# Performance work log

Hardware: AMD Instinct MI355X
Metric: run time of the kernel (lower is better)

Reference implementation:

```python
import jax, jax.numpy as jnp
import numpy as np

NUM_HEADS = 16
NEG_INF = -9e15


def setup_inputs() -> dict:
    key = jax.random.key(0)
    k1, k2, k3 = jax.random.split(key, 3)
    B, S, D = 2, 2048, 1024
    # xavier-uniform-ish init scale for weights
    lim_qkv = float(np.sqrt(6.0 / (D + 3 * D)))
    lim_o = float(np.sqrt(6.0 / (D + D)))
    return {
        "x": jax.random.normal(k1, (B, S, D), dtype=jnp.float32),
        "w_qkv": jax.random.uniform(k2, (3 * D, D), minval=-lim_qkv, maxval=lim_qkv, dtype=jnp.float32),
        "b_qkv": jnp.zeros((3 * D,), dtype=jnp.float32),
        "w_o": jax.random.uniform(k3, (D, D), minval=-lim_o, maxval=lim_o, dtype=jnp.float32),
        "b_o": jnp.zeros((D,), dtype=jnp.float32),
    }


def reference(x, w_qkv, b_qkv, w_o, b_o):
    B, S, D = x.shape
    H = NUM_HEADS
    hd = D // H
    # qkv projection: [B,S,3D]
    qkv = x @ w_qkv.T + b_qkv
    # -> [B, H, S, 3*hd], then split
    qkv = qkv.reshape(B, S, H, 3 * hd).transpose(0, 2, 1, 3)
    q, k, v = jnp.split(qkv, 3, axis=-1)  # each [B,H,S,hd]
    scale = 1.0 / jnp.sqrt(jnp.asarray(hd, dtype=x.dtype))
    logits = jnp.einsum("bhqd,bhkd->bhqk", q, k) * scale
    attn = jax.nn.softmax(logits, axis=-1)
    vals = jnp.einsum("bhqk,bhkd->bhqd", attn, v)
    vals = vals.transpose(0, 2, 1, 3).reshape(B, S, D)
    return vals @ w_o.T + b_o
```

## Files before the change

kernel.cpp:

```cpp
#include <hip/hip_runtime.h>
#include <math.h>

#define NHEADS 16
#define HD 64

typedef __attribute__((ext_vector_type(8))) _Float16 half8;
typedef __attribute__((ext_vector_type(4))) _Float16 half4;
typedef __attribute__((ext_vector_type(4))) float f32x4;
typedef __attribute__((ext_vector_type(16))) float f32x16;
typedef __attribute__((ext_vector_type(4))) unsigned int u32x4;

__device__ inline void load_lds16(const void* g, void* l) {
    __builtin_amdgcn_global_load_lds(
        (const __attribute__((address_space(1))) unsigned int*)g,
        (__attribute__((address_space(3))) unsigned int*)l, 16, 0, 0);
}
__device__ inline void pl32swap(unsigned int& x, unsigned int& y) {
    asm volatile("v_permlane32_swap_b32 %0, %1" : "+v"(x), "+v"(y));
}

#define NX  4194304
#define NWQ 3145728
#define NWO 1048576
__global__ void cvt_all(const float* __restrict__ x, const float* __restrict__ wq,
                        const float* __restrict__ wo, _Float16* __restrict__ xf,
                        _Float16* __restrict__ wqf, _Float16* __restrict__ wof) {
    int i = (blockIdx.x * blockDim.x + threadIdx.x) * 8;
    const float* src; _Float16* dst; int off;
    if (i < NX)            { src = x;  dst = xf;  off = i; }
    else if (i < NX + NWQ) { src = wq; dst = wqf; off = i - NX; }
    else                   { src = wo; dst = wof; off = i - (NX + NWQ); }
    float4 a = *(const float4*)(src + off);
    float4 b = *(const float4*)(src + off + 4);
    half8 h;
    h[0] = (_Float16)a.x; h[1] = (_Float16)a.y; h[2] = (_Float16)a.z; h[3] = (_Float16)a.w;
    h[4] = (_Float16)b.x; h[5] = (_Float16)b.y; h[6] = (_Float16)b.z; h[7] = (_Float16)b.w;
    *(half8*)(dst + off) = h;
}

#define QSCALE 0.18033688f
__global__ __launch_bounds__(512, 2) void gemm_qkv(
    const _Float16* __restrict__ A, const _Float16* __restrict__ B,
    const float* __restrict__ bias,
    _Float16* __restrict__ Qf, _Float16* __restrict__ Kf,
    _Float16* __restrict__ VfT) {
    __shared__ __align__(1024) unsigned char smem[114688];
    const int tid = threadIdx.x;
    const int l = tid & 63, w = tid >> 6;
    const int wr = w >> 2, wc = w & 3;
    const int col16 = l & 15, kc = l >> 4;
    const int bid = blockIdx.y * gridDim.x + blockIdx.x;
    const int swz = (bid & 7) * 32 + (bid >> 3);
    const int m0 = (swz >> 4) * 256, n0 = (swz & 15) * 192;

    const int srcRow = w * 8 + (l >> 3);
    const int srcChunk = ((l & 7) ^ (l >> 3)) * 8;
    size_t aSrc[4], bSrc[3];
    #pragma unroll
    for (int q = 0; q < 4; ++q)
        aSrc[q] = (size_t)(m0 + q * 64 + srcRow) * 1024 + srcChunk;
    #pragma unroll
    for (int q = 0; q < 3; ++q)
        bSrc[q] = (size_t)(n0 + q * 64 + srcRow) * 1024 + srcChunk;
    const int ldsLane = w * 1024;

    const int swzl = col16 & 7;
    const int chOff0 = ((kc) ^ swzl) << 4;
    const int chOff1 = ((4 + kc) ^ swzl) << 4;
    int rowA[8], rowB[3];
    #pragma unroll
    for (int f = 0; f < 8; ++f) rowA[f] = (wr * 128 + f * 16 + col16) * 128;
    #pragma unroll
    for (int g = 0; g < 3; ++g) rowB[g] = (wc * 48 + g * 16 + col16) * 128;

    f32x4 acc[8][3] = {};

#define SU_A(q_, tt_) load_lds16(A + aSrc[q_] + (tt_) * 64, \
        smem + ((tt_) & 1) * 32768 + (q_) * 8192 + ldsLane);
#define SU_B(q_, tt_) load_lds16(B + bSrc[q_] + (tt_) * 64, \
        smem + 65536 + ((tt_) & 1) * 24576 + (q_) * 8192 + ldsLane);

#define VMW2 asm volatile("s_waitcnt vmcnt(2)" ::: "memory");
#define VMW3 asm volatile("s_waitcnt vmcnt(3)" ::: "memory");
#define VMW0 asm volatile("s_waitcnt vmcnt(0)" ::: "memory");

#define PH(mh_, g0_, gn_, bufA_, bufB_, VMWSTMT, STAGES) { \
    VMWSTMT \
    __builtin_amdgcn_sched_barrier(0); \
    __builtin_amdgcn_s_barrier(); \
    __builtin_amdgcn_sched_barrier(0); \
    half8 af[4][2], bf[gn_][2]; \
    _Pragma("unroll") \
    for (int f = 0; f < 4; ++f) { \
        const unsigned char* ap = smem + (bufA_) + rowA[(mh_) * 4 + f]; \
        af[f][0] = *(const half8*)(ap + chOff0); \
        af[f][1] = *(const half8*)(ap + chOff1); \
    } \
    _Pragma("unroll") \
    for (int g = 0; g < (gn_); ++g) { \
        const unsigned char* bp = smem + (bufB_) + rowB[(g0_) + g]; \
        bf[g][0] = *(const half8*)(bp + chOff0); \
        bf[g][1] = *(const half8*)(bp + chOff1); \
    } \
    STAGES \
    asm volatile("s_waitcnt lgkmcnt(0)" ::: "memory"); \
    __builtin_amdgcn_sched_barrier(0); \
    __builtin_amdgcn_s_setprio(1); \
    _Pragma("unroll") \
    for (int f = 0; f < 4; ++f) \
        _Pragma("unroll") \
        for (int g = 0; g < (gn_); ++g) { \
            acc[(mh_) * 4 + f][(g0_) + g] = __builtin_amdgcn_mfma_f32_16x16x32_f16( \
                af[f][0], bf[g][0], acc[(mh_) * 4 + f][(g0_) + g], 0, 0, 0); \
            acc[(mh_) * 4 + f][(g0_) + g] = __builtin_amdgcn_mfma_f32_16x16x32_f16( \
                af[f][1], bf[g][1], acc[(mh_) * 4 + f][(g0_) + g], 0, 0, 0); \
        } \
    __builtin_amdgcn_s_setprio(0); }

    SU_B(0, 0) SU_B(1, 0) SU_B(2, 0)
    SU_A(0, 0) SU_A(2, 0) SU_A(1, 0) SU_A(3, 0)

    for (int t = 0; t < 15; ++t) {
        const int bufA = (t & 1) * 32768;
        const int bufB = 65536 + (t & 1) * 24576;
        PH(0, 0, 2, bufA, bufB, VMW2, { SU_B(0, t + 1) SU_B(1, t + 1) })
        PH(0, 2, 1, bufA, bufB, ,     { SU_B(2, t + 1) })
        PH(1, 0, 2, bufA, bufB, VMW3, { SU_A(0, t + 1) SU_A(2, t + 1) })
        PH(1, 2, 1, bufA, bufB, ,     { SU_A(1, t + 1) SU_A(3, t + 1) })
    }
    PH(0, 0, 2, 32768, 65536 + 24576, VMW2, {})
    PH(0, 2, 1, 32768, 65536 + 24576, ,     {})
    PH(1, 0, 2, 32768, 65536 + 24576, VMW0, {})
    PH(1, 2, 1, 32768, 65536 + 24576, ,     {})

#undef SU_A
#undef SU_B
#undef VMW2
#undef VMW3
#undef VMW0
#undef PH

    const int rowb = m0 + wr * 128 + (l >> 4) * 4;
    const int colb = n0 + wc * 48 + col16;
    #pragma unroll
    for (int n = 0; n < 3; ++n) {
        int col = colb + n * 16;
        int h = col / 192;
        int rem = col - h * 192;
        int part = rem >> 6, d = rem & 63;
        float bv = bias[col];
        #pragma unroll
        for (int m = 0; m < 8; ++m) {
            int r0 = rowb + m * 16;
            int b = r0 >> 11, s0r = r0 & 2047;
            int bh = b * 16 + h;
            if (part == 0) {
                #pragma unroll
                for (int j = 0; j < 4; ++j)
                    Qf[((size_t)bh * 2048 + s0r + j) * 64 + d] =
                        (_Float16)((acc[m][n][j] + bv) * QSCALE);
            } else if (part == 1) {
                #pragma unroll
                for (int j = 0; j < 4; ++j)
                    Kf[((size_t)bh * 2048 + s0r + j) * 64 + d] = (_Float16)(acc[m][n][j] + bv);
            } else {
                half4 pk;
                pk[0] = (_Float16)(acc[m][n][0] + bv);
                pk[1] = (_Float16)(acc[m][n][1] + bv);
                pk[2] = (_Float16)(acc[m][n][2] + bv);
                pk[3] = (_Float16)(acc[m][n][3] + bv);
                *(half4*)&VfT[((size_t)bh * 64 + d) * 2048 + s0r] = pk;
            }
        }
    }
}

__global__ __launch_bounds__(256, 2) void gemm_o(
    const _Float16* __restrict__ A, const _Float16* __restrict__ B,
    const float* __restrict__ bias, float* __restrict__ C,
    int M, int N, int K) {
    __shared__ __align__(1024) unsigned char smem[36864];
    const int tid = threadIdx.x;
    const int l = tid & 63, w = tid >> 6;
    const int wr = w >> 1, wc = w & 1;
    const int nwg = gridDim.x * gridDim.y;
    const int bid = blockIdx.y * gridDim.x + blockIdx.x;
    const int swz = (bid & 7) * (nwg >> 3) + (bid >> 3);
    const int m0 = (swz / gridDim.x) * 128, n0 = (swz % gridDim.x) * 64;
    const int srow = tid >> 2;
    const int schunk = (tid & 3) ^ ((srow >> 1) & 3);
    const size_t gA0 = (size_t)(m0 + srow) * K + schunk * 8;
    const size_t gA1 = gA0 + (size_t)64 * K;
    const size_t gB0 = (size_t)(n0 + srow) * K + schunk * 8;
    unsigned char* ldsW = smem + w * 1024;
    const int col16 = l & 15, kc = l >> 4;
    const int ra0 = wr * 64 + col16;
    const int offA = ra0 * 64 + ((kc ^ ((ra0 >> 1) & 3)) * 16);
    const int rb0 = wc * 32 + col16;
    const int offB = rb0 * 64 + ((kc ^ ((rb0 >> 1) & 3)) * 16);
    f32x4 acc[4][2] = {};

#define OSTAGE(k0_, buf_)                                                              \
    load_lds16(A + gA0 + (k0_), ldsW + (buf_) * 12288 + 0);                            \
    load_lds16(A + gA1 + (k0_), ldsW + (buf_) * 12288 + 4096);                         \
    load_lds16(B + gB0 + (k0_), ldsW + (buf_) * 12288 + 8192);
#define OSTEP(s_, buf_, VM, dostage)                                                   \
    asm volatile("s_waitcnt " VM ::: "memory");                                        \
    __builtin_amdgcn_sched_barrier(0);                                                 \
    __builtin_amdgcn_s_barrier();                                                      \
    if (dostage) { OSTAGE(((s_) + 2) * 32, ((buf_) + 2) % 3) }                         \
    {                                                                                  \
        const unsigned char* bs = smem + (buf_) * 12288;                               \
        half8 af[4], bf[2];                                                            \
        _Pragma("unroll")                                                              \
        for (int m = 0; m < 4; ++m) af[m] = *(const half8*)(bs + offA + m * 1024);     \
        _Pragma("unroll")                                                              \
        for (int n = 0; n < 2; ++n) bf[n] = *(const half8*)(bs + 8192 + offB + n * 1024); \
        _Pragma("unroll")                                                              \
        for (int m = 0; m < 4; ++m)                                                    \
            _Pragma("unroll")                                                          \
            for (int n = 0; n < 2; ++n)                                                \
                acc[m][n] = __builtin_amdgcn_mfma_f32_16x16x32_f16(af[m], bf[n], acc[m][n], 0, 0, 0); \
    }

    OSTAGE(0, 0)
    OSTAGE(32, 1)
    for (int t = 0; t < 30; t += 3) {
        OSTEP(t, 0, "vmcnt(3)", 1)
        OSTEP(t + 1, 1, "vmcnt(3)", 1)
        OSTEP(t + 2, 2, "vmcnt(3)", 1)
    }
    OSTEP(30, 0, "vmcnt(3)", 0)
    OSTEP(31, 1, "vmcnt(0)", 0)
#undef OSTAGE
#undef OSTEP

    const int rowb = m0 + wr * 64 + (l >> 4) * 4;
    const int colb = n0 + wc * 32 + col16;
    float bv[2];
    #pragma unroll
    for (int n = 0; n < 2; ++n) bv[n] = bias[colb + n * 16];
    #pragma unroll
    for (int m = 0; m < 4; ++m)
        #pragma unroll
        for (int j = 0; j < 4; ++j) {
            float* crow = C + (size_t)(rowb + m * 16 + j) * N + colb;
            #pragma unroll
            for (int n = 0; n < 2; ++n) crow[n * 16] = acc[m][n][j] + bv[n];
        }
}

__global__ __launch_bounds__(512, 2) void mfma_attn(
    const _Float16* __restrict__ Qf, const _Float16* __restrict__ Kf,
    const _Float16* __restrict__ VfT, _Float16* __restrict__ vals) {
    __shared__ __align__(1024) unsigned char smem[49152];
    const int tid = threadIdx.x;
    const int l = tid & 63, w = tid >> 6;
    const int l31 = l & 31, hl = l >> 5;
    const int hwbid = blockIdx.y * gridDim.x + blockIdx.x;
    const int q_t = (hwbid >> 3) & 7;
    const int bh = (hwbid & 7) + ((hwbid >> 6) << 3);
    const int q0 = q_t * 256;
    const int h = bh & 15, b = bh >> 4;

    half8 qf[4];
    {
        const _Float16* qp = Qf + ((size_t)bh * 2048 + q0 + w * 32 + l31) * 64 + hl * 8;
        #pragma unroll
        for (int c = 0; c < 4; ++c) qf[c] = *(const half8*)(qp + c * 16);
    }
    f32x16 zvec = {};
    f32x16 o0 = {}, o1 = {};
    float mshift = 0.f, lsum = 0.f;

    const _Float16* Kg = Kf + (size_t)bh * 2048 * 64;
    const _Float16* Vg = VfT + (size_t)bh * 64 * 2048;

    int offK, offV;
    {
        int row2 = w * 4 + (l >> 4);
        int slot = (l & 15) ^ (row2 & 15);
        int row = row2 * 2 + (slot >> 3);
        int chunk = slot & 7;
        offK = row * 64 + chunk * 8;
        offV = row * 2048 + chunk * 8;
    }
    const int sbase = (l31 & 1) * 8;
    const int xr = (l31 >> 1) & 15;
    const int rb0 = (l31 >> 1) * 256;

    #define STAGE(kt0, buf)                                                            \
        {                                                                              \
            unsigned char* bK = smem + (buf) * 8192 + w * 1024;                        \
            unsigned char* bV = smem + 24576 + (buf) * 8192 + w * 1024;                \
            load_lds16(Kg + (size_t)(kt0) * 64 + offK, bK);                            \
            load_lds16(Vg + (kt0) + offV, bV);                                         \
        }

    #define QK_TILE(kb, D0, D1)                                                        \
        {                                                                              \
            const unsigned char* Ksb_ = smem + (kb) * 8192;                            \
            {                                                                          \
                int chOff = ((sbase + hl) ^ xr) << 4;                                  \
                half8 k0_ = *(const half8*)(Ksb_ + rb0 + chOff);                       \
                half8 k1_ = *(const half8*)(Ksb_ + rb0 + 4096 + chOff);                \
                D0 = __builtin_amdgcn_mfma_f32_32x32x16_f16(k0_, qf[0], zvec, 0, 0, 0);\
                D1 = __builtin_amdgcn_mfma_f32_32x32x16_f16(k1_, qf[0], zvec, 0, 0, 0);\
            }                                                                          \
            _Pragma("unroll")                                                          \
            for (int kcq = 1; kcq < 4; ++kcq) {                                        \
                int chOff = ((sbase + kcq * 2 + hl) ^ xr) << 4;                        \
                half8 k0_ = *(const half8*)(Ksb_ + rb0 + chOff);                       \
                half8 k1_ = *(const half8*)(Ksb_ + rb0 + 4096 + chOff);                \
                D0 = __builtin_amdgcn_mfma_f32_32x32x16_f16(k0_, qf[kcq], D0, 0, 0, 0);\
                D1 = __builtin_amdgcn_mfma_f32_32x32x16_f16(k1_, qf[kcq], D1, 0, 0, 0);\
            }                                                                          \
        }

    #define SMPV(S0, S1, vb_)                                                          \
        {                                                                              \
            const unsigned char* Vsb_ = smem + 24576 + (vb_) * 8192;                   \
            if (__any(mshift != 0.f)) {                                                \
                _Pragma("unroll")                                                      \
                for (int r = 0; r < 16; ++r) { S0[r] -= mshift; S1[r] -= mshift; }     \
            }                                                                          \
            float r0 = 0.f, r1 = 0.f, r2 = 0.f, r3 = 0.f;                              \
            unsigned int a[2][8];                                                      \
            _Pragma("unroll")                                                          \
            for (int j = 0; j < 8; ++j) {                                              \
                float p0 = __builtin_amdgcn_exp2f(S0[2 * j]);                          \
                float p1 = __builtin_amdgcn_exp2f(S0[2 * j + 1]);                      \
                float q0_ = __builtin_amdgcn_exp2f(S1[2 * j]);                         \
                float q1_ = __builtin_amdgcn_exp2f(S1[2 * j + 1]);                     \
                r0 += p0; r1 += p1; r2 += q0_; r3 += q1_;                              \
                a[0][j] = __builtin_bit_cast(unsigned int, __builtin_amdgcn_cvt_pkrtz(p0, p1));   \
                a[1][j] = __builtin_bit_cast(unsigned int, __builtin_amdgcn_cvt_pkrtz(q0_, q1_)); \
            }                                                                          \
            float rsum = (r0 + r1) + (r2 + r3);                                        \
            if (__any(rsum > 32768.f)) {                                               \
                float pmax = S0[0];                                                    \
                _Pragma("unroll")                                                      \
                for (int r = 1; r < 16; ++r) pmax = fmaxf(pmax, S0[r]);                \
                _Pragma("unroll")                                                      \
                for (int r = 0; r < 16; ++r) pmax = fmaxf(pmax, S1[r]);                \
                pmax = fmaxf(pmax, __shfl_xor(pmax, 32, 64));                          \
                float d_ = fmaxf(pmax, 0.f);                                           \
                float corr = __builtin_amdgcn_exp2f(-d_);                              \
                _Pragma("unroll")                                                      \
                for (int r = 0; r < 16; ++r) { S0[r] -= d_; S1[r] -= d_; }             \
                _Pragma("unroll")                                                      \
                for (int r = 0; r < 16; ++r) { o0[r] *= corr; o1[r] *= corr; }         \
                lsum *= corr;                                                          \
                mshift += d_;                                                          \
                r0 = r1 = r2 = r3 = 0.f;                                               \
                _Pragma("unroll")                                                      \
                for (int j = 0; j < 8; ++j) {                                          \
                    float p0 = __builtin_amdgcn_exp2f(S0[2 * j]);                      \
                    float p1 = __builtin_amdgcn_exp2f(S0[2 * j + 1]);                  \
                    float q0_ = __builtin_amdgcn_exp2f(S1[2 * j]);                     \
                    float q1_ = __builtin_amdgcn_exp2f(S1[2 * j + 1]);                 \
                    r0 += p0; r1 += p1; r2 += q0_; r3 += q1_;                          \
                    a[0][j] = __builtin_bit_cast(unsigned int, __builtin_amdgcn_cvt_pkrtz(p0, p1));   \
                    a[1][j] = __builtin_bit_cast(unsigned int, __builtin_amdgcn_cvt_pkrtz(q0_, q1_)); \
                }                                                                      \
                rsum = (r0 + r1) + (r2 + r3);                                          \
            }                                                                          \
            lsum += rsum;                                                              \
            _Pragma("unroll")                                                          \
            for (int c = 0; c < 2; ++c) {                                              \
                pl32swap(a[c][0], a[c][2]);                                            \
                pl32swap(a[c][1], a[c][3]);                                            \
                pl32swap(a[c][4], a[c][6]);                                            \
                pl32swap(a[c][5], a[c][7]);                                            \
            }                                                                          \
            _Pragma("unroll")                                                          \
            for (int kk = 0; kk < 4; ++kk) {                                           \
                u32x4 pw;                                                              \
                pw.x = a[kk >> 1][(kk & 1) * 4 + 0];                                   \
                pw.y = a[kk >> 1][(kk & 1) * 4 + 1];                                   \
                pw.z = a[kk >> 1][(kk & 1) * 4 + 2];                                   \
                pw.w = a[kk >> 1][(kk & 1) * 4 + 3];                                   \
                half8 pf = __builtin_bit_cast(half8, pw);                              \
                int chOff = ((sbase + kk * 2 + hl) ^ xr) << 4;                         \
                half8 v0 = *(const half8*)(Vsb_ + rb0 + chOff);                        \
                half8 v1 = *(const half8*)(Vsb_ + rb0 + 4096 + chOff);                 \
                o0 = __builtin_amdgcn_mfma_f32_32x32x16_f16(v0, pf, o0, 0, 0, 0);      \
                o1 = __builtin_amdgcn_mfma_f32_32x32x16_f16(v1, pf, o1, 0, 0, 0);      \
            }                                                                          \
        }

    #define AITER(tt, kb, VM, dostage)                                                 \
        asm volatile("s_waitcnt " VM ::: "memory");                                    \
        __builtin_amdgcn_sched_barrier(0);                                             \
        __builtin_amdgcn_s_barrier();                                                  \
        if (dostage) STAGE(((tt) + 2) * 64, ((kb) + 2) % 3)                            \
        QK_TILE(kb, sS0, sS1)                                                          \
        SMPV(sS0, sS1, kb)

    STAGE(0, 0)
    STAGE(64, 1)
    f32x16 sS0, sS1;
    for (int t = 0; t < 30; t += 3) {
        AITER(t, 0, "vmcnt(2)", 1)
        AITER(t + 1, 1, "vmcnt(2)", 1)
        AITER(t + 2, 2, "vmcnt(2)", 1)
    }
    AITER(30, 0, "vmcnt(2)", 0)
    AITER(31, 1, "vmcnt(0)", 0)

    lsum += __shfl_xor(lsum, 32, 64);
    float inv = 1.f / lsum;
    size_t orow = ((size_t)(b * 2048 + q0 + w * 32 + l31)) * 1024 + h * 64;
    #pragma unroll
    for (int dc = 0; dc < 2; ++dc) {
        const f32x16* op = dc ? &o1 : &o0;
        #pragma unroll
        for (int rq = 0; rq < 4; ++rq) {
            int d0 = dc * 32 + rq * 8 + hl * 4;
            half4 hv;
            #pragma unroll
            for (int j = 0; j < 4; ++j) hv[j] = (_Float16)((*op)[rq * 4 + j] * inv);
            *(half4*)(vals + orow + d0) = hv;
        }
    }
}

extern "C" void kernel_launch(void* const* d_in, const int* in_sizes, int n_in,
                              void* d_out, int out_size, void* d_ws, size_t ws_size,
                              hipStream_t stream) {
    const float* x     = (const float*)d_in[0];
    const float* w_qkv = (const float*)d_in[1];
    const float* b_qkv = (const float*)d_in[2];
    const float* w_o   = (const float*)d_in[3];
    const float* b_o   = (const float*)d_in[4];
    float* out = (float*)d_out;

    const int B = 2, S = 2048, D = 1024;
    const int M = B * S;
    const int N1 = 3 * D;
    const int BH = B * NHEADS;

    _Float16* xf  = (_Float16*)d_ws;
    _Float16* wqf = xf  + (size_t)M * D;
    _Float16* wof = wqf + (size_t)N1 * D;
    _Float16* Qf  = wof + (size_t)D * D;
    _Float16* Kf  = Qf  + (size_t)BH * S * HD;
    _Float16* VfT = Kf  + (size_t)BH * S * HD;
    _Float16* vals = xf;

    cvt_all<<<(NX + NWQ + NWO) / 2048, 256, 0, stream>>>(x, w_qkv, w_o, xf, wqf, wof);

    gemm_qkv<<<dim3(16, 16), 512, 0, stream>>>(xf, wqf, b_qkv, Qf, Kf, VfT);

    mfma_attn<<<dim3(S / 256, BH), 512, 0, stream>>>(Qf, Kf, VfT, vals);

    gemm_o<<<dim3(D / 64, M / 128), 256, 0, stream>>>(vals, wof, b_o, out, M, D, D);
}
```

Before: 102.0 us.

## Process two query sub-tiles per wave in attention, halving block threads

Each wave in the attention kernel now handles 64 query rows (two 32-row groups) instead of 32, and the block shrinks from 512 to 256 threads while still covering 256 queries. Every K and V fragment read from LDS now feeds twice as many MFMAs, which cuts LDS read traffic per FLOP. Each thread issues twice as many async global-to-LDS loads per stage, and the vmcnt waits change to match. The cost is higher register pressure from doubled accumulators and softmax state, and fewer waves per CU to hide latency.

```diff
diff --git a/kernel.cpp b/kernel.cpp
--- a/kernel.cpp
+++ b/kernel.cpp
@@ -250,7 +250,7 @@
         }
 }
 
-__global__ __launch_bounds__(512, 2) void mfma_attn(
+__global__ __launch_bounds__(256, 2) void mfma_attn(
     const _Float16* __restrict__ Qf, const _Float16* __restrict__ Kf,
     const _Float16* __restrict__ VfT, _Float16* __restrict__ vals) {
     __shared__ __align__(1024) unsigned char smem[49152];
@@ -263,27 +263,31 @@
     const int q0 = q_t * 256;
     const int h = bh & 15, b = bh >> 4;
 
-    half8 qf[4];
+    half8 qfA[4], qfB[4];
     {
-        const _Float16* qp = Qf + ((size_t)bh * 2048 + q0 + w * 32 + l31) * 64 + hl * 8;
+        const _Float16* qp = Qf + ((size_t)bh * 2048 + q0 + w * 64 + l31) * 64 + hl * 8;
         #pragma unroll
-        for (int c = 0; c < 4; ++c) qf[c] = *(const half8*)(qp + c * 16);
+        for (int c = 0; c < 4; ++c) qfA[c] = *(const half8*)(qp + c * 16);
+        qp += (size_t)32 * 64;
+        #pragma unroll
+        for (int c = 0; c < 4; ++c) qfB[c] = *(const half8*)(qp + c * 16);
     }
     f32x16 zvec = {};
-    f32x16 o0 = {}, o1 = {};
-    float mshift = 0.f, lsum = 0.f;
+    f32x16 oA0 = {}, oA1 = {}, oB0 = {}, oB1 = {};
+    float msA = 0.f, msB = 0.f, lsA = 0.f, lsB = 0.f;
 
     const _Float16* Kg = Kf + (size_t)bh * 2048 * 64;
     const _Float16* Vg = VfT + (size_t)bh * 64 * 2048;
 
-    int offK, offV;
-    {
-        int row2 = w * 4 + (l >> 4);
+    int offK[2], offV[2];
+    #pragma unroll
+    for (int i = 0; i < 2; ++i) {
+        int row2 = w * 8 + i * 4 + (l >> 4);
         int slot = (l & 15) ^ (row2 & 15);
         int row = row2 * 2 + (slot >> 3);
         int chunk = slot & 7;
-        offK = row * 64 + chunk * 8;
-        offV = row * 2048 + chunk * 8;
+        offK[i] = row * 64 + chunk * 8;
+        offV[i] = row * 2048 + chunk * 8;
     }
     const int sbase = (l31 & 1) * 8;
     const int xr = (l31 >> 1) & 15;
@@ -291,41 +295,45 @@
 
     #define STAGE(kt0, buf)                                                            \
         {                                                                              \
-            unsigned char* bK = smem + (buf) * 8192 + w * 1024;                        \
-            unsigned char* bV = smem + 24576 + (buf) * 8192 + w * 1024;                \
-            load_lds16(Kg + (size_t)(kt0) * 64 + offK, bK);                            \
-            load_lds16(Vg + (kt0) + offV, bV);                                         \
-        }
-
-    #define QK_TILE(kb, D0, D1)                                                        \
+            unsigned char* bK = smem + (buf) * 16384 + w * 2048;                       \
+            unsigned char* bV = bK + 8192;                                             \
+            load_lds16(Kg + (size_t)(kt0) * 64 + offK[0], bK);                         \
+            load_lds16(Kg + (size_t)(kt0) * 64 + offK[1], bK + 1024);                  \
+            load_lds16(Vg + (kt0) + offV[0], bV);                                      \
+            load_lds16(Vg + (kt0) + offV[1], bV + 1024);                               \
+        }
+
+    #define QK2(slot_)                                                                 \
         {                                                                              \
-            const unsigned char* Ksb_ = smem + (kb) * 8192;                            \
+            const unsigned char* Ksb_ = smem + (slot_) * 16384;                        \
             {                                                                          \
                 int chOff = ((sbase + hl) ^ xr) << 4;                                  \
                 half8 k0_ = *(const half8*)(Ksb_ + rb0 + chOff);                       \
                 half8 k1_ = *(const half8*)(Ksb_ + rb0 + 4096 + chOff);                \
-                D0 = __builtin_amdgcn_mfma_f32_32x32x16_f16(k0_, qf[0], zvec, 0, 0, 0);\
-                D1 = __builtin_amdgcn_mfma_f32_32x32x16_f16(k1_, qf[0], zvec, 0, 0, 0);\
+                sA0 = __builtin_amdgcn_mfma_f32_32x32x16_f16(k0_, qfA[0], zvec, 0, 0, 0); \
+                sA1 = __builtin_amdgcn_mfma_f32_32x32x16_f16(k1_, qfA[0], zvec, 0, 0, 0); \
+                sB0 = __builtin_amdgcn_mfma_f32_32x32x16_f16(k0_, qfB[0], zvec, 0, 0, 0); \
+                sB1 = __builtin_amdgcn_mfma_f32_32x32x16_f16(k1_, qfB[0], zvec, 0, 0, 0); \
             }                                                                          \
             _Pragma("unroll")                                                          \
-            for (int kcq = 1; kcq < 4; ++kcq) {                                        \
-                int chOff = ((sbase + kcq * 2 + hl) ^ xr) << 4;                        \
+            for (int kc = 1; kc < 4; ++kc) {                                           \
+                int chOff = ((sbase + kc * 2 + hl) ^ xr) << 4;                         \
                 half8 k0_ = *(const half8*)(Ksb_ + rb0 + chOff);                       \
                 half8 k1_ = *(const half8*)(Ksb_ + rb0 + 4096 + chOff);                \
-                D0 = __builtin_amdgcn_mfma_f32_32x32x16_f16(k0_, qf[kcq], D0, 0, 0, 0);\
-                D1 = __builtin_amdgcn_mfma_f32_32x32x16_f16(k1_, qf[kcq], D1, 0, 0, 0);\
-            }                                                                          \
-        }
-
-    #define SMPV(S0, S1, vb_)                                                          \
+                sA0 = __builtin_amdgcn_mfma_f32_32x32x16_f16(k0_, qfA[kc], sA0, 0, 0, 0); \
+                sA1 = __builtin_amdgcn_mfma_f32_32x32x16_f16(k1_, qfA[kc], sA1, 0, 0, 0); \
+                sB0 = __builtin_amdgcn_mfma_f32_32x32x16_f16(k0_, qfB[kc], sB0, 0, 0, 0); \
+                sB1 = __builtin_amdgcn_mfma_f32_32x32x16_f16(k1_, qfB[kc], sB1, 0, 0, 0); \
+            }                                                                          \
+        }
+
+    #define SM_G(S0, S1, O0, O1, AA, ls_, ms_)                                         \
         {                                                                              \
-            const unsigned char* Vsb_ = smem + 24576 + (vb_) * 8192;                   \
-            if (__any(mshift != 0.f)) {                                                \
-                _Pragma("unroll")                                                      \
-                for (int r = 0; r < 16; ++r) { S0[r] -= mshift; S1[r] -= mshift; }     \
+            if (__any(ms_ != 0.f)) {                                                   \
+                _Pragma("unroll")                                                      \
+                for (int r = 0; r < 16; ++r) { S0[r] -= ms_; S1[r] -= ms_; }           \
             }                                                                          \
             float r0 = 0.f, r1 = 0.f, r2 = 0.f, r3 = 0.f;                              \
-            unsigned int a[2][8];                                                      \
             _Pragma("unroll")                                                          \
             for (int j = 0; j < 8; ++j) {                                              \
                 float p0 = __builtin_amdgcn_exp2f(S0[2 * j]);                          \
@@ -333,8 +341,8 @@
                 float q0_ = __builtin_amdgcn_exp2f(S1[2 * j]);                         \
                 float q1_ = __builtin_amdgcn_exp2f(S1[2 * j + 1]);                     \
                 r0 += p0; r1 += p1; r2 += q0_; r3 += q1_;                              \
-                a[0][j] = __builtin_bit_cast(unsigned int, __builtin_amdgcn_cvt_pkrtz(p0, p1));   \
-                a[1][j] = __builtin_bit_cast(unsigned int, __builtin_amdgcn_cvt_pkrtz(q0_, q1_)); \
+                AA[0][j] = __builtin_bit_cast(unsigned int, __builtin_amdgcn_cvt_pkrtz(p0, p1));   \
+                AA[1][j] = __builtin_bit_cast(unsigned int, __builtin_amdgcn_cvt_pkrtz(q0_, q1_)); \
             }                                                                          \
             float rsum = (r0 + r1) + (r2 + r3);                                        \
             if (__any(rsum > 32768.f)) {                                               \
@@ -349,9 +357,9 @@
                 _Pragma("unroll")                                                      \
                 for (int r = 0; r < 16; ++r) { S0[r] -= d_; S1[r] -= d_; }             \
                 _Pragma("unroll")                                                      \
-                for (int r = 0; r < 16; ++r) { o0[r] *= corr; o1[r] *= corr; }         \
-                lsum *= corr;                                                          \
-                mshift += d_;                                                          \
+                for (int r = 0; r < 16; ++r) { O0[r] *= corr; O1[r] *= corr; }         \
+                ls_ *= corr;                                                           \
+                ms_ += d_;                                                             \
                 r0 = r1 = r2 = r3 = 0.f;                                               \
                 _Pragma("unroll")                                                      \
                 for (int j = 0; j < 8; ++j) {                                          \
@@ -360,32 +368,44 @@
                     float q0_ = __builtin_amdgcn_exp2f(S1[2 * j]);                     \
                     float q1_ = __builtin_amdgcn_exp2f(S1[2 * j + 1]);                 \
                     r0 += p0; r1 += p1; r2 += q0_; r3 += q1_;                          \
-                    a[0][j] = __builtin_bit_cast(unsigned int, __builtin_amdgcn_cvt_pkrtz(p0, p1));   \
-                    a[1][j] = __builtin_bit_cast(unsigned int, __builtin_amdgcn_cvt_pkrtz(q0_, q1_)); \
+                    AA[0][j] = __builtin_bit_cast(unsigned int, __builtin_amdgcn_cvt_pkrtz(p0, p1));   \
+                    AA[1][j] = __builtin_bit_cast(unsigned int, __builtin_amdgcn_cvt_pkrtz(q0_, q1_)); \
                 }                                                                      \
                 rsum = (r0 + r1) + (r2 + r3);                                          \
             }                                                                          \
-            lsum += rsum;                                                              \
+            ls_ += rsum;                                                               \
             _Pragma("unroll")                                                          \
             for (int c = 0; c < 2; ++c) {                                              \
-                pl32swap(a[c][0], a[c][2]);                                            \
-                pl32swap(a[c][1], a[c][3]);                                            \
-                pl32swap(a[c][4], a[c][6]);                                            \
-                pl32swap(a[c][5], a[c][7]);                                            \
-            }                                                                          \
+                pl32swap(AA[c][0], AA[c][2]);                                          \
+                pl32swap(AA[c][1], AA[c][3]);                                          \
+                pl32swap(AA[c][4], AA[c][6]);                                          \
+                pl32swap(AA[c][5], AA[c][7]);                                          \
+            }                                                                          \
+        }
+
+    #define PV2(slot_)                                                                 \
+        {                                                                              \
+            const unsigned char* Vsb_ = smem + (slot_) * 16384 + 8192;                 \
             _Pragma("unroll")                                                          \
             for (int kk = 0; kk < 4; ++kk) {                                           \
-                u32x4 pw;                                                              \
-                pw.x = a[kk >> 1][(kk & 1) * 4 + 0];                                   \
-                pw.y = a[kk >> 1][(kk & 1) * 4 + 1];                                   \
-                pw.z = a[kk >> 1][(kk & 1) * 4 + 2];                                   \
-                pw.w = a[kk >> 1][(kk & 1) * 4 + 3];                                   \
-                half8 pf = __builtin_bit_cast(half8, pw);                              \
+                u32x4 pwA, pwB;                                                        \
+                pwA.x = aA[kk >> 1][(kk & 1) * 4 + 0];                                 \
+                pwA.y = aA[kk >> 1][(kk & 1) * 4 + 1];                                 \
+                pwA.z = aA[kk >> 1][(kk & 1) * 4 + 2];                                 \
+                pwA.w = aA[kk >> 1][(kk & 1) * 4 + 3];                                 \
+                pwB.x = aB[kk >> 1][(kk & 1) * 4 + 0];                                 \
+                pwB.y = aB[kk >> 1][(kk & 1) * 4 + 1];                                 \
+                pwB.z = aB[kk >> 1][(kk & 1) * 4 + 2];                                 \
+                pwB.w = aB[kk >> 1][(kk & 1) * 4 + 3];                                 \
+                half8 pfA = __builtin_bit_cast(half8, pwA);                            \
+                half8 pfB = __builtin_bit_cast(half8, pwB);                            \
                 int chOff = ((sbase + kk * 2 + hl) ^ xr) << 4;                         \
                 half8 v0 = *(const half8*)(Vsb_ + rb0 + chOff);                        \
                 half8 v1 = *(const half8*)(Vsb_ + rb0 + 4096 + chOff);                 \
-                o0 = __builtin_amdgcn_mfma_f32_32x32x16_f16(v0, pf, o0, 0, 0, 0);      \
-                o1 = __builtin_amdgcn_mfma_f32_32x32x16_f16(v1, pf, o1, 0, 0, 0);      \
+                oA0 = __builtin_amdgcn_mfma_f32_32x32x16_f16(v0, pfA, oA0, 0, 0, 0);   \
+                oA1 = __builtin_amdgcn_mfma_f32_32x32x16_f16(v1, pfA, oA1, 0, 0, 0);   \
+                oB0 = __builtin_amdgcn_mfma_f32_32x32x16_f16(v0, pfB, oB0, 0, 0, 0);   \
+                oB1 = __builtin_amdgcn_mfma_f32_32x32x16_f16(v1, pfB, oB1, 0, 0, 0);   \
             }                                                                          \
         }
 
@@ -394,33 +414,45 @@
         __builtin_amdgcn_sched_barrier(0);                                             \
         __builtin_amdgcn_s_barrier();                                                  \
         if (dostage) STAGE(((tt) + 2) * 64, ((kb) + 2) % 3)                            \
-        QK_TILE(kb, sS0, sS1)                                                          \
-        SMPV(sS0, sS1, kb)
+        QK2(kb)                                                                        \
+        {                                                                              \
+            unsigned int aA[2][8], aB[2][8];                                           \
+            SM_G(sA0, sA1, oA0, oA1, aA, lsA, msA)                                     \
+            SM_G(sB0, sB1, oB0, oB1, aB, lsB, msB)                                     \
+            PV2(kb)                                                                    \
+        }
 
     STAGE(0, 0)
     STAGE(64, 1)
-    f32x16 sS0, sS1;
+    f32x16 sA0, sA1, sB0, sB1;
     for (int t = 0; t < 30; t += 3) {
-        AITER(t, 0, "vmcnt(2)", 1)
-        AITER(t + 1, 1, "vmcnt(2)", 1)
-        AITER(t + 2, 2, "vmcnt(2)", 1)
-    }
-    AITER(30, 0, "vmcnt(2)", 0)
+        AITER(t, 0, "vmcnt(4)", 1)
+        AITER(t + 1, 1, "vmcnt(4)", 1)
+        AITER(t + 2, 2, "vmcnt(4)", 1)
+    }
+    AITER(30, 0, "vmcnt(4)", 0)
     AITER(31, 1, "vmcnt(0)", 0)
 
-    lsum += __shfl_xor(lsum, 32, 64);
-    float inv = 1.f / lsum;
-    size_t orow = ((size_t)(b * 2048 + q0 + w * 32 + l31)) * 1024 + h * 64;
+    lsA += __shfl_xor(lsA, 32, 64);
+    lsB += __shfl_xor(lsB, 32, 64);
+    float invA = 1.f / lsA, invB = 1.f / lsB;
+    size_t orowA = ((size_t)(b * 2048 + q0 + w * 64 + l31)) * 1024 + h * 64;
+    size_t orowB = orowA + (size_t)32 * 1024;
     #pragma unroll
     for (int dc = 0; dc < 2; ++dc) {
-        const f32x16* op = dc ? &o1 : &o0;
+        const f32x16* opA = dc ? &oA1 : &oA0;
+        const f32x16* opB = dc ? &oB1 : &oB0;
         #pragma unroll
         for (int rq = 0; rq < 4; ++rq) {
             int d0 = dc * 32 + rq * 8 + hl * 4;
-            half4 hv;
+            half4 hvA, hvB;
             #pragma unroll
-            for (int j = 0; j < 4; ++j) hv[j] = (_Float16)((*op)[rq * 4 + j] * inv);
-            *(half4*)(vals + orow + d0) = hv;
+            for (int j = 0; j < 4; ++j) {
+                hvA[j] = (_Float16)((*opA)[rq * 4 + j] * invA);
+                hvB[j] = (_Float16)((*opB)[rq * 4 + j] * invB);
+            }
+            *(half4*)(vals + orowA + d0) = hvA;
+            *(half4*)(vals + orowB + d0) = hvB;
         }
     }
 }
@@ -452,7 +484,7 @@
 
     gemm_qkv<<<dim3(16, 16), 512, 0, stream>>>(xf, wqf, b_qkv, Qf, Kf, VfT);
 
-    mfma_attn<<<dim3(S / 256, BH), 512, 0, stream>>>(Qf, Kf, VfT, vals);
+    mfma_attn<<<dim3(S / 256, BH), 256, 0, stream>>>(Qf, Kf, VfT, vals);
 
     gemm_o<<<dim3(D / 64, M / 128), 256, 0, stream>>>(vals, wof, b_o, out, M, D, D);
 }
```

New measurement: 103.8 us. No clear change (+1.7%).
